# Kernel optimization log

Hardware: AMD Instinct MI355X
Metric: run time of the kernel (lower is better)

Reference implementation:

```python
import jax, jax.numpy as jnp
import numpy as np

K = 100
TEMPERATURE = 1.0


def setup_inputs() -> dict:
    key = jax.random.key(0)
    k1, k2, k3 = jax.random.split(key, 3)
    student_emb = jax.random.normal(k1, (8, 512, 1500), dtype=jnp.float32)
    teacher_codes = jax.random.randint(k2, (8, 1500), 0, 4096, dtype=jnp.int64)
    codebook = jax.random.normal(k3, (4096, 512), dtype=jnp.float32)
    return {"student_emb": student_emb, "teacher_codes": teacher_codes, "codebook": codebook}


def reference(student_emb, teacher_codes, codebook):
    B, C, T = student_emb.shape
    # flatten tokens: (N, C) with N = B*T
    emb = jnp.transpose(student_emb, (0, 2, 1)).reshape(-1, C)
    codes = teacher_codes.reshape(-1).astype(jnp.int32)

    # Euclidean cdist via the ||a||^2 + ||b||^2 - 2ab expansion (same math as torch.cdist)
    emb_sq = jnp.sum(emb * emb, axis=1, keepdims=True)            # (N,1)
    cb_sq = jnp.sum(codebook * codebook, axis=1)[None, :]         # (1,V)
    d2 = emb_sq + cb_sq - 2.0 * jnp.matmul(emb, codebook.T)       # (N,V)
    distances = jnp.sqrt(jnp.maximum(d2, 0.0))

    # top-k smallest distances
    _, top_k_indices = jax.lax.top_k(-distances, K)               # (N,K)

    # include_correct: replace last candidate with the true code if absent
    correct_in_topk = jnp.any(top_k_indices == codes[:, None], axis=1)
    top_k_indices = top_k_indices.at[:, -1].set(
        jnp.where(correct_in_topk, top_k_indices[:, -1], codes))

    candidate_distances = jnp.take_along_axis(distances, top_k_indices, axis=1)
    logits = -candidate_distances / TEMPERATURE                   # (N,K)

    match = top_k_indices == codes[:, None]
    local_labels = jnp.argmax(match.astype(jnp.int32), axis=1)    # (N,)

    logp = jax.nn.log_softmax(logits, axis=1)
    loss = -jnp.mean(jnp.take_along_axis(logp, local_labels[:, None], axis=1))

    local_predictions = jnp.argmax(logits, axis=-1)
    local_accuracy = jnp.mean((local_predictions == local_labels).astype(jnp.float32))
    global_predictions = jnp.argmin(distances, axis=-1)
    global_accuracy = jnp.mean((global_predictions == codes).astype(jnp.float32))
    correct_in_candidates = jnp.mean(jnp.any(top_k_indices == codes[:, None], axis=1).astype(jnp.float32))

    return loss, local_accuracy, global_accuracy, correct_in_candidates
```

## Files before the change

### kernel.cpp

```cpp
#include <hip/hip_runtime.h>
#include <hip/hip_bf16.h>
#include <cstdint>

#define B_ 8
#define C_ 512
#define T_ 1500
#define N_ (B_*T_)
#define NPAD_ 12032
#define V_ 4096
#define K_ 100

typedef unsigned long long u64;
typedef __attribute__((ext_vector_type(8))) short short8;
typedef __attribute__((ext_vector_type(8))) unsigned short u16x8;
typedef __attribute__((ext_vector_type(4))) float f32x4;

__device__ __forceinline__ unsigned short f2bf(float x){
    __hip_bfloat16 h = __float2bfloat16(x);
    return __builtin_bit_cast(unsigned short, h);
}
__device__ __forceinline__ unsigned short f2h(float x){
    return __builtin_bit_cast(unsigned short, (_Float16)x);
}
__device__ __forceinline__ float h2f(unsigned short h){
    return (float)__builtin_bit_cast(_Float16, h);
}

__device__ __forceinline__ void gll16(const unsigned short* g, unsigned short* l){
    __builtin_amdgcn_global_load_lds(
        (const __attribute__((address_space(1))) void*)g,
        (__attribute__((address_space(3))) void*)l, 16, 0, 0);
}

__global__ __launch_bounds__(256) void cbconv_kernel(const float* __restrict__ CB,
                                                     unsigned short* __restrict__ CBh,
                                                     float* __restrict__ csq){
    int wv = threadIdx.x >> 6, lane = threadIdx.x & 63;
    int r = blockIdx.x * 4 + wv;
    const float4* p4 = (const float4*)(CB + (size_t)r * C_);
    ushort4* o4 = (ushort4*)(CBh + (size_t)r * C_);
    float s = 0.f;
    #pragma unroll
    for (int j = 0; j < 2; ++j){
        float4 v = p4[lane + j*64];
        s += v.x*v.x + v.y*v.y + v.z*v.z + v.w*v.w;
        ushort4 h; h.x = f2bf(v.x); h.y = f2bf(v.y); h.z = f2bf(v.z); h.w = f2bf(v.w);
        o4[lane + j*64] = h;
    }
    #pragma unroll
    for (int o = 32; o; o >>= 1) s += __shfl_down(s, o, 64);
    if (lane == 0) csq[r] = s;
}

__global__ __launch_bounds__(256) void transpose_conv_kernel(const float* __restrict__ S,
                                                             unsigned short* __restrict__ embT,
                                                             float* __restrict__ esq){
    __shared__ float tile[32][33];
    __shared__ float psum[8][33];
    int b  = blockIdx.z;
    int c0 = blockIdx.y * 32;
    int t0 = blockIdx.x * 32;
    int tx = threadIdx.x, ty = threadIdx.y;
    #pragma unroll
    for (int r = 0; r < 4; ++r){
        int c = c0 + ty + r*8;
        int t = t0 + tx;
        tile[ty + r*8][tx] = (t < T_) ? S[((size_t)b*C_ + c)*T_ + t] : 0.f;
    }
    __syncthreads();
    float ps = 0.f;
    #pragma unroll
    for (int r = 0; r < 4; ++r){ float v = tile[ty + r*8][tx]; ps += v * v; }
    psum[ty][tx] = ps;
    #pragma unroll
    for (int r = 0; r < 4; ++r){
        int t = t0 + ty + r*8;
        int c = c0 + tx;
        if (t < T_) embT[((size_t)b*T_ + t)*C_ + c] = f2bf(tile[tx][ty + r*8]);
    }
    __syncthreads();
    if (ty == 0){
        int t = t0 + tx;
        if (t < T_){
            float s2 = 0.f;
            #pragma unroll
            for (int w = 0; w < 8; ++w) s2 += psum[w][tx];
            atomicAdd(&esq[b*T_ + t], s2);
        }
    }
}

__global__ __launch_bounds__(256) void gemm_dot_kernel(
    const unsigned short* __restrict__ A, const unsigned short* __restrict__ Bm,
    unsigned short* __restrict__ doth, int row_lo, int row_hi)
{
    __shared__ unsigned short smem[128*136];
    unsigned short* As = smem;
    unsigned short* Bs = smem + 128*32;
    int tid = threadIdx.x, lane = tid & 63, wv = tid >> 6;
    int row0 = row_lo + blockIdx.x * 128;
    int col0 = blockIdx.y * 128;

    int sr = lane >> 2;
    int sk = (lane & 3) * 8;
    int ar0 = row0 + wv*32 + sr;       int ar1 = ar0 + 16;
    int ca0 = (ar0 < N_) ? ar0 : N_-1; int ca1 = (ar1 < N_) ? ar1 : N_-1;
    const unsigned short* Ap0 = A  + (size_t)ca0 * C_ + sk;
    const unsigned short* Ap1 = A  + (size_t)ca1 * C_ + sk;
    const unsigned short* Bp0 = Bm + (size_t)(col0 + wv*32 + sr) * C_ + sk;
    const unsigned short* Bp1 = Bp0 + (size_t)16 * C_;
    unsigned short* Ad0 = &As[(wv*32     ) * 32];
    unsigned short* Ad1 = &As[(wv*32 + 16) * 32];
    unsigned short* Bd0 = &Bs[(wv*32     ) * 32];
    unsigned short* Bd1 = &Bs[(wv*32 + 16) * 32];

    int wm = (wv >> 1) * 64, wn = (wv & 1) * 64;
    int fr = lane & 15;
    int fk = (lane >> 4) * 8;

    f32x4 acc[4][4];
    #pragma unroll
    for (int i = 0; i < 4; ++i)
        #pragma unroll
        for (int j = 0; j < 4; ++j) acc[i][j] = (f32x4){0.f, 0.f, 0.f, 0.f};

    for (int kt = 0; kt < C_/32; ++kt){
        int k0 = kt * 32;
        gll16(Ap0 + k0, Ad0);
        gll16(Ap1 + k0, Ad1);
        gll16(Bp0 + k0, Bd0);
        gll16(Bp1 + k0, Bd1);
        __syncthreads();
        short8 af[4], bf[4];
        #pragma unroll
        for (int i = 0; i < 4; ++i) af[i] = *(const short8*)&As[(wm + i*16 + fr)*32 + fk];
        #pragma unroll
        for (int j = 0; j < 4; ++j) bf[j] = *(const short8*)&Bs[(wn + j*16 + fr)*32 + fk];
        #pragma unroll
        for (int i = 0; i < 4; ++i)
            #pragma unroll
            for (int j = 0; j < 4; ++j)
                acc[i][j] = __builtin_amdgcn_mfma_f32_16x16x32_bf16(bf[j], af[i], acc[i][j], 0, 0, 0);
        __syncthreads();
    }

    const int LD = 136;
    int en = lane & 15;
    int ev = (lane >> 4) * 4;
    #pragma unroll
    for (int i = 0; i < 4; ++i){
        int r = wm + i*16 + en;
        #pragma unroll
        for (int j = 0; j < 4; ++j){
            ushort4 h;
            h.x = f2h(acc[i][j][0]);
            h.y = f2h(acc[i][j][1]);
            h.z = f2h(acc[i][j][2]);
            h.w = f2h(acc[i][j][3]);
            *(ushort4*)&smem[r*LD + wn + j*16 + ev] = h;
        }
    }
    __syncthreads();

    int rr = tid >> 4;
    int cc = (tid & 15) * 8;
    #pragma unroll
    for (int it = 0; it < 8; ++it){
        int r = it*16 + rr;
        int n = row0 + r;
        if (n < row_hi){
            u16x8 v = *(const u16x8*)&smem[r*LD + cc];
            *(u16x8*)&doth[(size_t)(n - row_lo) * V_ + col0 + cc] = v;
        }
    }
}

__global__ __launch_bounds__(256, 2) void select_kernel(const unsigned short* __restrict__ doth,
                                                        const int* __restrict__ codes,
                                                        const float* __restrict__ esq,
                                                        const float* __restrict__ csq,
                                                        float2* __restrict__ pairbuf,
                                                        int row_lo, int nrows){
    int tid = threadIdx.x, lane = tid & 63, wv = tid >> 6;
    int lrow = blockIdx.x * 4 + wv;
    if (lrow >= nrows) return;
    int n = row_lo + lrow;
    const u16x8* r8 = (const u16x8*)(doth + (size_t)lrow * V_);

    __shared__ unsigned hist[4][256] __attribute__((aligned(16)));
    __shared__ unsigned coll[4][64];
    __shared__ unsigned collcnt[4];

    float esq_n = esq[n];
    int code = codes[n];
    float dotc = h2f(doth[(size_t)lrow * V_ + code]);
    unsigned ucode = __float_as_uint(fmaxf(esq_n + csq[code] - 2.f * dotc, 0.f));

    unsigned u[64];
    #pragma unroll
    for (int j = 0; j < 8; ++j){
        u16x8 h = r8[lane + j*64];
        const float4* cp = (const float4*)(csq + 8*lane + 512*j);
        float4 c0 = cp[0], c1 = cp[1];
        float cs[8] = {c0.x, c0.y, c0.z, c0.w, c1.x, c1.y, c1.z, c1.w};
        #pragma unroll
        for (int e = 0; e < 8; ++e){
            float d2 = fmaxf(esq_n + cs[e] - 2.f * h2f(h[e]), 0.f);
            u[8*j+e] = __float_as_uint(d2);
        }
    }

    unsigned umin = u[0], umax = u[0];
    #pragma unroll
    for (int k = 1; k < 64; ++k){
        umin = (u[k] < umin) ? u[k] : umin;
        umax = (u[k] > umax) ? u[k] : umax;
    }
    #pragma unroll
    for (int o = 32; o; o >>= 1){
        unsigned a = (unsigned)__shfl_xor((int)umin, o, 64); if (a < umin) umin = a;
        unsigned b = (unsigned)__shfl_xor((int)umax, o, 64); if (b > umax) umax = b;
    }
    unsigned im = 0xFFFFFFFFu;
    #pragma unroll
    for (int k = 0; k < 64; ++k){
        unsigned idx = 8u*(unsigned)lane + (unsigned)(512*(k >> 3) + (k & 7));
        if (u[k] == umin && idx < im) im = idx;
    }
    #pragma unroll
    for (int o = 32; o; o >>= 1){
        unsigned a = (unsigned)__shfl_xor((int)im, o, 64); if (a < im) im = a;
    }
    int idx0 = (int)im;
    float d0 = sqrtf(__uint_as_float(umin));

    unsigned t;
    if (umin == umax){
        t = umin;
    } else {
        ((uint4*)&hist[wv][0])[lane] = (uint4){0u,0u,0u,0u};
        if (lane == 0) collcnt[wv] = 0u;
        asm volatile("s_waitcnt lgkmcnt(0)" ::: "memory");
        float fmn = __uint_as_float(umin), fmx = __uint_as_float(umax);
        float invw = 256.0f / (fmx - fmn);
        #pragma unroll
        for (int k = 0; k < 64; ++k){
            float fk = __uint_as_float(u[k]);
            int b = (int)((fk - fmn) * invw); b = (b > 255) ? 255 : b;
            atomicAdd(&hist[wv][b], 1u);
        }
        asm volatile("s_waitcnt lgkmcnt(0)" ::: "memory");
        uint4 hq = ((uint4*)&hist[wv][0])[lane];
        unsigned lsum = hq.x + hq.y + hq.z + hq.w;
        unsigned inc = lsum;
        #pragma unroll
        for (int o = 1; o < 64; o <<= 1){
            unsigned y = (unsigned)__shfl_up((int)inc, o, 64);
            if (lane >= o) inc += y;
        }
        unsigned e0 = inc - lsum;
        unsigned e1 = e0 + hq.x, e2 = e1 + hq.y, e3 = e2 + hq.z, e4 = e3 + hq.w;
        int sel = -1;
        if      (e0 <= 99u && 99u < e1) sel = 0;
        else if (e1 <= 99u && 99u < e2) sel = 1;
        else if (e2 <= 99u && 99u < e3) sel = 2;
        else if (e3 <= 99u && 99u < e4) sel = 3;
        u64 bal = __ballot(sel >= 0);
        int src = __ffsll(bal) - 1;
        unsigned myBk = (unsigned)(4*lane + (sel < 0 ? 0 : sel));
        unsigned myBase = (sel == 1) ? e1 : (sel == 2) ? e2 : (sel == 3) ? e3 : e0;
        int Bk   = __shfl((int)myBk,   src, 64);
        int base = __shfl((int)myBase, src, 64);
        int rk = 99 - base;
        #pragma unroll
        for (int k = 0; k < 64; ++k){
            float fk = __uint_as_float(u[k]);
            int b = (int)((fk - fmn) * invw); b = (b > 255) ? 255 : b;
            if (b == Bk){
                unsigned pos = atomicAdd(&collcnt[wv], 1u);
                if (pos < 64u) coll[wv][pos] = u[k];
            }
        }
        asm volatile("s_waitcnt lgkmcnt(0)" ::: "memory");
        unsigned bcnt = collcnt[wv];
        if (bcnt <= 64u){
            unsigned w = (lane < (int)bcnt) ? coll[wv][lane] : 0xFFFFFFFFu;
            unsigned wmn = (lane < (int)bcnt) ? w : 0xFFFFFFFFu;
            unsigned wmx = (lane < (int)bcnt) ? w : 0u;
            #pragma unroll
            for (int o = 32; o; o >>= 1){
                unsigned a = (unsigned)__shfl_xor((int)wmn, o, 64); if (a < wmn) wmn = a;
                unsigned b = (unsigned)__shfl_xor((int)wmx, o, 64); if (b > wmx) wmx = b;
            }
            unsigned P;
            if (wmn == wmx) P = wmn;
            else {
                int hb = 31 - __clz((int)(wmn ^ wmx));
                unsigned mask = (hb == 31) ? 0xFFFFFFFFu : ((1u << (hb+1)) - 1u);
                P = wmn & ~mask;
                for (int b = hb; b >= 0; --b){
                    unsigned cand = P | (1u << b);
                    int c = __popcll(__ballot(w < cand));
                    if (c <= rk) P = cand;
                }
            }
            t = P;
        } else {
            int hb = 31 - __clz((int)(umin ^ umax));
            unsigned mask = (hb == 31) ? 0xFFFFFFFFu : ((1u << (hb+1)) - 1u);
            unsigned P = umin & ~mask;
            for (int b = hb; b >= 0; --b){
                unsigned cand = P | (1u << b);
                int c = 0;
                #pragma unroll
                for (int k = 0; k < 64; ++k) c += (u[k] < cand) ? 1 : 0;
                #pragma unroll
                for (int o = 32; o; o >>= 1) c += __shfl_xor(c, o, 64);
                if (c <= 99) P = cand;
            }
            t = P;
        }
    }
    float tval = sqrtf(__uint_as_float(t));

    float s = 0.f; int cl = 0;
    #pragma unroll
    for (int k = 0; k < 64; ++k){
        if (u[k] < t){ s += __expf(d0 - sqrtf(__uint_as_float(u[k]))); cl++; }
    }
    #pragma unroll
    for (int o = 32; o; o >>= 1){
        s += __shfl_xor(s, o, 64);
        cl += __shfl_xor(cl, o, 64);
    }
    if (lane == 0){
        float S = s + (float)(K_ - cl) * __expf(d0 - tval);
        float dcode = sqrtf(__uint_as_float(ucode));
        if (ucode > t) S += __expf(d0 - dcode) - __expf(d0 - tval);
        float nll = dcode - d0 + __logf(S);
        pairbuf[n] = make_float2(nll, (idx0 == code) ? 1.f : 0.f);
    }
}

__global__ __launch_bounds__(1024) void finalize_kernel(const float2* __restrict__ pair,
                                                        float* __restrict__ out){
    int tid = threadIdx.x;
    float sn = 0.f, sh = 0.f;
    for (int i = tid; i < N_; i += 1024){
        float2 p = pair[i]; sn += p.x; sh += p.y;
    }
    #pragma unroll
    for (int o = 32; o; o >>= 1){ sn += __shfl_down(sn, o, 64); sh += __shfl_down(sh, o, 64); }
    __shared__ float a[16], b[16];
    int wv = tid >> 6, lane = tid & 63;
    if (lane == 0){ a[wv] = sn; b[wv] = sh; }
    __syncthreads();
    if (tid == 0){
        float L = 0.f, H = 0.f;
        #pragma unroll
        for (int i = 0; i < 16; ++i){ L += a[i]; H += b[i]; }
        out[0] = L / (float)N_;
        out[1] = H / (float)N_;
        out[2] = H / (float)N_;
        out[3] = 1.0f;
    }
}

extern "C" void kernel_launch(void* const* d_in, const int* in_sizes, int n_in,
                              void* d_out, int out_size, void* d_ws, size_t ws_size,
                              hipStream_t stream){
    const float* S   = (const float*)d_in[0];
    const int* codes = (const int*)d_in[1];
    const float* CB  = (const float*)d_in[2];
    float* out = (float*)d_out;

    char* w = (char*)d_ws;
    size_t off = 0;
    unsigned short* embT = (unsigned short*)(w + off); off += (size_t)NPAD_ * C_ * 2;
    unsigned short* CBh  = (unsigned short*)(w + off); off += (size_t)V_ * C_ * 2;
    float* csq = (float*)(w + off); off += (size_t)V_ * 4;
    float* esq = (float*)(w + off); off += (size_t)N_ * 4;
    off = (off + 255) & ~(size_t)255;
    float2* pairbuf = (float2*)(w + off); off += (size_t)N_ * 8;
    unsigned short* dotbuf = (unsigned short*)(w + off);

    size_t avail = (ws_size > off) ? ws_size - off : 0;
    long maxrows = (long)(avail / ((size_t)V_ * 2));
    int chunk = (maxrows >= N_) ? N_ : (int)maxrows;
    if (chunk < 4) chunk = 4;

    hipMemsetAsync(esq, 0, (size_t)N_ * 4, stream);
    hipLaunchKernelGGL(cbconv_kernel, dim3(V_/4), dim3(256), 0, stream, CB, CBh, csq);
    hipLaunchKernelGGL(transpose_conv_kernel, dim3((T_+31)/32, C_/32, B_), dim3(32, 8), 0, stream,
                       S, embT, esq);

    for (int row_lo = 0; row_lo < N_; row_lo += chunk){
        int row_hi = row_lo + chunk; if (row_hi > N_) row_hi = N_;
        int rows = row_hi - row_lo;
        hipLaunchKernelGGL(gemm_dot_kernel, dim3((rows + 127)/128, V_/128), dim3(256), 0, stream,
                           embT, CBh, dotbuf, row_lo, row_hi);
        hipLaunchKernelGGL(select_kernel, dim3((rows + 3)/4), dim3(256), 0, stream,
                           dotbuf, codes, esq, csq, pairbuf, row_lo, rows);
    }
    hipLaunchKernelGGL(finalize_kernel, dim3(1), dim3(1024), 0, stream, pairbuf, out);
}
```

Baseline: 218.7 us.

## Deepen GEMM K-tile to 64 with XOR-swizzled LDS and XCD-aware block remap

The bf16 MFMA GEMM now stages a K-depth of 64 per iteration instead of 32, which halves the number of barrier pairs and global-to-LDS rounds. The LDS rows are XOR-swizzled by row to avoid bank conflicts on the wider rows. Workgroup IDs are remapped so consecutive logical tiles land on the same XCD, which is meant to improve L2 reuse. LDS usage per tile doubles, though it still fits in the existing 128x136 buffer.

```diff
diff --git a/kernel.cpp b/kernel.cpp
--- a/kernel.cpp
+++ b/kernel.cpp
@@ -96,27 +96,42 @@
 {
     __shared__ unsigned short smem[128*136];
     unsigned short* As = smem;
-    unsigned short* Bs = smem + 128*32;
+    unsigned short* Bs = smem + 128*64;
     int tid = threadIdx.x, lane = tid & 63, wv = tid >> 6;
-    int row0 = row_lo + blockIdx.x * 128;
-    int col0 = blockIdx.y * 128;
-
-    int sr = lane >> 2;
-    int sk = (lane & 3) * 8;
-    int ar0 = row0 + wv*32 + sr;       int ar1 = ar0 + 16;
-    int ca0 = (ar0 < N_) ? ar0 : N_-1; int ca1 = (ar1 < N_) ? ar1 : N_-1;
-    const unsigned short* Ap0 = A  + (size_t)ca0 * C_ + sk;
-    const unsigned short* Ap1 = A  + (size_t)ca1 * C_ + sk;
-    const unsigned short* Bp0 = Bm + (size_t)(col0 + wv*32 + sr) * C_ + sk;
-    const unsigned short* Bp1 = Bp0 + (size_t)16 * C_;
-    unsigned short* Ad0 = &As[(wv*32     ) * 32];
-    unsigned short* Ad1 = &As[(wv*32 + 16) * 32];
-    unsigned short* Bd0 = &Bs[(wv*32     ) * 32];
-    unsigned short* Bd1 = &Bs[(wv*32 + 16) * 32];
+
+    int nbx = gridDim.x;
+    int hw  = blockIdx.x + nbx * blockIdx.y;
+    int nwg = nbx * gridDim.y;
+    int lg  = hw;
+    if ((nwg & 7) == 0){
+        int per = nwg >> 3;
+        lg = (hw & 7) * per + (hw >> 3);
+    }
+    int bx = lg % nbx, by = lg / nbx;
+    int row0 = row_lo + bx * 128;
+    int col0 = by * 128;
+
+    int rb = wv*8 + (lane >> 3);
+    int ke = (((lane & 7) ^ ((lane >> 3) & 7)) << 3);
+
+    const unsigned short* ApS[4];
+    const unsigned short* BpS[4];
+    unsigned short* Adst[4];
+    unsigned short* Bdst[4];
+    #pragma unroll
+    for (int p = 0; p < 4; ++p){
+        int ra = row0 + p*32 + rb;
+        int ca = (ra < N_) ? ra : N_-1;
+        ApS[p] = A  + (size_t)ca * C_ + ke;
+        BpS[p] = Bm + (size_t)(col0 + p*32 + rb) * C_ + ke;
+        Adst[p] = &As[p*2048 + wv*512];
+        Bdst[p] = &Bs[p*2048 + wv*512];
+    }
 
     int wm = (wv >> 1) * 64, wn = (wv & 1) * 64;
-    int fr = lane & 15;
-    int fk = (lane >> 4) * 8;
+    int fr  = lane & 15;
+    int fko = (lane >> 4) * 8;
+    int sx  = (fr & 7) << 3;
 
     f32x4 acc[4][4];
     #pragma unroll
@@ -124,23 +139,27 @@
         #pragma unroll
         for (int j = 0; j < 4; ++j) acc[i][j] = (f32x4){0.f, 0.f, 0.f, 0.f};
 
-    for (int kt = 0; kt < C_/32; ++kt){
-        int k0 = kt * 32;
-        gll16(Ap0 + k0, Ad0);
-        gll16(Ap1 + k0, Ad1);
-        gll16(Bp0 + k0, Bd0);
-        gll16(Bp1 + k0, Bd1);
+    for (int kt = 0; kt < C_/64; ++kt){
+        int k0 = kt * 64;
+        #pragma unroll
+        for (int p = 0; p < 4; ++p) gll16(ApS[p] + k0, Adst[p]);
+        #pragma unroll
+        for (int p = 0; p < 4; ++p) gll16(BpS[p] + k0, Bdst[p]);
         __syncthreads();
-        short8 af[4], bf[4];
-        #pragma unroll
-        for (int i = 0; i < 4; ++i) af[i] = *(const short8*)&As[(wm + i*16 + fr)*32 + fk];
-        #pragma unroll
-        for (int j = 0; j < 4; ++j) bf[j] = *(const short8*)&Bs[(wn + j*16 + fr)*32 + fk];
-        #pragma unroll
-        for (int i = 0; i < 4; ++i)
+        #pragma unroll
+        for (int ks = 0; ks < 2; ++ks){
+            int kc = (ks*32 + fko) ^ sx;
+            short8 af[4], bf[4];
             #pragma unroll
-            for (int j = 0; j < 4; ++j)
-                acc[i][j] = __builtin_amdgcn_mfma_f32_16x16x32_bf16(bf[j], af[i], acc[i][j], 0, 0, 0);
+            for (int i = 0; i < 4; ++i) af[i] = *(const short8*)&As[(wm + i*16 + fr)*64 + kc];
+            #pragma unroll
+            for (int j = 0; j < 4; ++j) bf[j] = *(const short8*)&Bs[(wn + j*16 + fr)*64 + kc];
+            #pragma unroll
+            for (int i = 0; i < 4; ++i)
+                #pragma unroll
+                for (int j = 0; j < 4; ++j)
+                    acc[i][j] = __builtin_amdgcn_mfma_f32_16x16x32_bf16(bf[j], af[i], acc[i][j], 0, 0, 0);
+        }
         __syncthreads();
     }
 
```

Result: slower. 230.0 us (+5.1%).
